# Kernel tuning notes

Measured on AMD Instinct MI355X. Metric: run time of the kernel, lower is better.

Reference implementation:

```python
import jax, jax.numpy as jnp
import numpy as np

KERNEL = 3
PAD = (KERNEL - 1) // 2
KA = KERNEL * KERNEL          # kernel_area = 9
CENTER = KA // 2              # 4
CH_OUT = 64


def setup_inputs() -> dict:
    key = jax.random.key(0)
    k1, k2 = jax.random.split(key)
    x = jax.random.normal(k1, (8, 64, 128, 128), dtype=jnp.float32)
    weight = jax.random.uniform(k2, (1, 1, KA, 1, 1), dtype=jnp.float32)
    bias = jnp.zeros((1, 1, KA, 1, 1), dtype=jnp.float32)
    weight_center = jnp.ones((), dtype=jnp.float32)
    weight_median = jnp.ones((), dtype=jnp.float32)
    return {"x": x, "weight": weight, "bias": bias,
            "weight_center": weight_center, "weight_median": weight_median}


def _unfold_same(x):
    # x: (B, C, H, W) -> patches (B, C, KA, H, W), stride 1, zero pad
    B, C, H, W = x.shape
    xp = jnp.pad(x, ((0, 0), (0, 0), (PAD, PAD), (PAD, PAD)))
    # order matches F.unfold: index = ki*K + kj
    views = [xp[:, :, i:i + H, j:j + W] for i in range(KERNEL) for j in range(KERNEL)]
    return jnp.stack(views, axis=2)


def reference(x, weight, bias, weight_center, weight_median):
    B, C, H, W = x.shape
    x_sig = jax.nn.sigmoid(x)
    patches = _unfold_same(x_sig)                      # (B, C, KA, H, W)
    w = jax.nn.sigmoid(weight)
    b = jax.nn.sigmoid(bias)
    D = jnp.maximum(w, patches) + b                    # (B, C, KA, H, W)
    max_stat = jnp.sum(D, axis=2)
    # torch.median returns the lower middle element -> sort and index (KA-1)//2
    median_stat = jnp.sort(D, axis=2)[:, :, (KA - 1) // 2]
    mean_stat = jnp.mean(D, axis=2)
    center = patches[:, :, CENTER]
    out = (weight_center * center + weight_median * median_stat
           - max_stat - mean_stat)                     # (B, C, H, W)
    # expand to ch_out then sum over C_in -> every output channel is identical
    s = jnp.sum(out, axis=1)                           # (B, H, W)
    return jnp.broadcast_to(s[:, None], (B, CH_OUT, H, W))
```

## Files before the change

kernel.cpp:

```cpp
#include <hip/hip_runtime.h>

#define BATCH  8
#define CH     64
#define H      128
#define W      128
#define HW     (H * W)
#define RS     8
#define CPW    2
#define NCHUNK (CH / CPW)
#define NSTRIP (H / RS)

typedef float vfloat2 __attribute__((ext_vector_type(2)));
typedef float vfloat4 __attribute__((ext_vector_type(4)));

__device__ __forceinline__ float sigmoidf_(float v) {
    return 1.0f / (1.0f + __expf(-v));
}

__device__ __forceinline__ float pixel_val(
    const float p0, const float p1, const float p2,
    const float p3, const float p4, const float p5,
    const float p6, const float p7, const float p8,
    const float* __restrict__ wk, const float* __restrict__ bk,
    const float wc, const float wm)
{
    float d[9];
    d[0] = fmaxf(wk[0], p0) + bk[0];
    d[1] = fmaxf(wk[1], p1) + bk[1];
    d[2] = fmaxf(wk[2], p2) + bk[2];
    d[3] = fmaxf(wk[3], p3) + bk[3];
    d[4] = fmaxf(wk[4], p4) + bk[4];
    d[5] = fmaxf(wk[5], p5) + bk[5];
    d[6] = fmaxf(wk[6], p6) + bk[6];
    d[7] = fmaxf(wk[7], p7) + bk[7];
    d[8] = fmaxf(wk[8], p8) + bk[8];
    float sum = ((d[0] + d[1]) + (d[2] + d[3])) + ((d[5] + d[6]) + (d[7] + d[8])) + d[4];

    #define S2(a,bb) { float t = d[a]; d[a] = fminf(d[a], d[bb]); d[bb] = fmaxf(t, d[bb]); }
    S2(0,3) S2(1,4) S2(2,5) S2(0,1) S2(0,2) S2(4,5) S2(3,5)
    S2(1,2) S2(3,4) S2(1,3) S2(1,6) S2(4,6) S2(2,6)
    S2(2,3) S2(4,7) S2(2,4) S2(3,7)
    S2(4,8) S2(3,8) S2(3,4)
    #undef S2

    return wc * p4 + wm * d[4] - sum - sum * (1.0f / 9.0f);
}

__global__ __launch_bounds__(256) void partial_kernel(
    const float* __restrict__ x,
    const float* __restrict__ weight,
    const float* __restrict__ bias,
    const float* __restrict__ wcp,
    const float* __restrict__ wmp,
    float* __restrict__ ws)
{
    const int tid   = threadIdx.x;
    const int lane  = tid & 63;
    const int strip = blockIdx.x * 4 + (tid >> 6);
    const int chnk  = blockIdx.y;
    const int c0    = chnk * CPW;
    const int b     = blockIdx.z;

    const int row0 = strip * RS;
    const int col  = 2 * lane;

    float wk[9], bk[9];
    #pragma unroll
    for (int k = 0; k < 9; ++k) {
        wk[k] = sigmoidf_(weight[k]);
        bk[k] = sigmoidf_(bias[k]);
    }
    const float wc = wcp[0];
    const float wm = wmp[0];

    vfloat2 raw[CPW][RS + 2];
    #pragma unroll
    for (int cc = 0; cc < CPW; ++cc) {
        const float* base = x + ((size_t)b * CH + c0 + cc) * HW + col;
        #pragma unroll
        for (int rr = 0; rr < RS + 2; ++rr) {
            const int r_  = row0 + rr - 1;
            const int rcl = min(max(r_, 0), H - 1);
            raw[cc][rr] = *(const vfloat2*)(base + rcl * W);
        }
    }

    vfloat2 acc[RS];
    #pragma unroll
    for (int j = 0; j < RS; ++j) acc[j] = (vfloat2)(0.0f);

    #define SIGROW(cc, rr, Lr, Ar, Br, Rr)                                    \
    {                                                                         \
        const int  r_  = row0 + (rr) - 1;                                     \
        const bool okr = (r_ >= 0) & (r_ < H);                                \
        vfloat2 v = raw[cc][rr];                                              \
        Ar = okr ? sigmoidf_(v.x) : 0.0f;                                     \
        Br = okr ? sigmoidf_(v.y) : 0.0f;                                     \
        float lf = __shfl_up(Br, 1);                                          \
        float rg = __shfl_down(Ar, 1);                                        \
        Lr = (lane == 0)  ? 0.0f : lf;                                        \
        Rr = (lane == 63) ? 0.0f : rg;                                        \
    }

    #pragma unroll
    for (int cc = 0; cc < CPW; ++cc) {
        float L0, A0, B0, R0, L1, A1, B1, R1, L2, A2, B2, R2;
        SIGROW(cc, 0, L0, A0, B0, R0);
        SIGROW(cc, 1, L1, A1, B1, R1);

        #pragma unroll
        for (int j = 0; j < RS; ++j) {
            SIGROW(cc, j + 2, L2, A2, B2, R2);

            acc[j].x += pixel_val(L0, A0, B0,
                                  L1, A1, B1,
                                  L2, A2, B2, wk, bk, wc, wm);
            acc[j].y += pixel_val(A0, B0, R0,
                                  A1, B1, R1,
                                  A2, B2, R2, wk, bk, wc, wm);

            L0 = L1; A0 = A1; B0 = B1; R0 = R1;
            L1 = L2; A1 = A2; B1 = B2; R1 = R2;
        }
    }
    #undef SIGROW

    float* op = ws + ((size_t)b * NCHUNK + chnk) * HW + (size_t)row0 * W + col;
    #pragma unroll
    for (int j = 0; j < RS; ++j)
        *(vfloat2*)(op + (size_t)j * W) = acc[j];
}

__global__ __launch_bounds__(256) void broadcast_kernel(
    const float* __restrict__ ws,
    float* __restrict__ out)
{
    const int g  = (blockIdx.x * 256 + threadIdx.x) * 4;
    const int b  = g >> 14;
    const int p  = g & (HW - 1);
    const int c0 = blockIdx.y * 16;

    const float* wsb = ws + (size_t)b * NCHUNK * HW + p;
    vfloat4 s = (vfloat4)(0.0f);
    #pragma unroll
    for (int k = 0; k < NCHUNK; ++k)
        s += *(const vfloat4*)(wsb + (size_t)k * HW);

    float* base = out + ((size_t)b * CH + c0) * HW + p;
    #pragma unroll
    for (int j = 0; j < 16; ++j)
        __builtin_nontemporal_store(s, (vfloat4*)(base + (size_t)j * HW));
}

extern "C" void kernel_launch(void* const* d_in, const int* in_sizes, int n_in,
                              void* d_out, int out_size, void* d_ws, size_t ws_size,
                              hipStream_t stream) {
    const float* x      = (const float*)d_in[0];
    const float* weight = (const float*)d_in[1];
    const float* bias   = (const float*)d_in[2];
    const float* wcp    = (const float*)d_in[3];
    const float* wmp    = (const float*)d_in[4];
    float* out = (float*)d_out;
    float* ws  = (float*)d_ws;

    dim3 grid1(NSTRIP / 4, NCHUNK, BATCH);
    partial_kernel<<<grid1, 256, 0, stream>>>(x, weight, bias, wcp, wmp, ws);

    dim3 grid2(BATCH * HW / (4 * 256), CH / 16);
    broadcast_kernel<<<grid2, 256, 0, stream>>>(ws, out);
}
```

Baseline: 111.6 us.

## Reduce channel partials in shared memory to shrink workspace traffic

Each 512-thread block now has 8 waves, each covering 4 channels over a 4-row strip. The per-wave partial sums are reduced across waves in LDS, so only 2 partial planes per batch go to the workspace instead of 32. This cuts workspace writes and the broadcast kernel's reads, and the broadcast grid is retuned to 8 channels per block. The cost is a block-wide sync, more halo rows reloaded and re-sigmoided per output row (6 loads for 4 rows versus 10 for 8), and higher register pressure from 4 channels of raw data per thread.

```diff
diff --git a/kernel.cpp b/kernel.cpp
--- a/kernel.cpp
+++ b/kernel.cpp
@@ -5,10 +5,10 @@
 #define H      128
 #define W      128
 #define HW     (H * W)
-#define RS     8
-#define CPW    2
-#define NCHUNK (CH / CPW)
-#define NSTRIP (H / RS)
+#define TH     4
+#define NSTRIP (H / TH)
+#define WAVES  8
+#define CPW    4
 
 typedef float vfloat2 __attribute__((ext_vector_type(2)));
 typedef float vfloat4 __attribute__((ext_vector_type(4)));
@@ -46,7 +46,7 @@
     return wc * p4 + wm * d[4] - sum - sum * (1.0f / 9.0f);
 }
 
-__global__ __launch_bounds__(256) void partial_kernel(
+__global__ __launch_bounds__(512) void partial_kernel(
     const float* __restrict__ x,
     const float* __restrict__ weight,
     const float* __restrict__ bias,
@@ -54,15 +54,18 @@
     const float* __restrict__ wmp,
     float* __restrict__ ws)
 {
-    const int tid   = threadIdx.x;
-    const int lane  = tid & 63;
-    const int strip = blockIdx.x * 4 + (tid >> 6);
-    const int chnk  = blockIdx.y;
-    const int c0    = chnk * CPW;
+    __shared__ float red[WAVES][TH][W];
+
+    const int tid  = threadIdx.x;
+    const int lane = tid & 63;
+    const int w    = tid >> 6;
+    const int strip = blockIdx.x;
+    const int half  = blockIdx.y;
     const int b     = blockIdx.z;
 
-    const int row0 = strip * RS;
+    const int row0 = strip * TH;
     const int col  = 2 * lane;
+    const int c0   = half * (WAVES * CPW) + w * CPW;
 
     float wk[9], bk[9];
     #pragma unroll
@@ -73,21 +76,21 @@
     const float wc = wcp[0];
     const float wm = wmp[0];
 
-    vfloat2 raw[CPW][RS + 2];
+    vfloat2 raw[CPW][TH + 2];
     #pragma unroll
     for (int cc = 0; cc < CPW; ++cc) {
         const float* base = x + ((size_t)b * CH + c0 + cc) * HW + col;
         #pragma unroll
-        for (int rr = 0; rr < RS + 2; ++rr) {
+        for (int rr = 0; rr < TH + 2; ++rr) {
             const int r_  = row0 + rr - 1;
             const int rcl = min(max(r_, 0), H - 1);
             raw[cc][rr] = *(const vfloat2*)(base + rcl * W);
         }
     }
 
-    vfloat2 acc[RS];
+    vfloat2 acc[TH];
     #pragma unroll
-    for (int j = 0; j < RS; ++j) acc[j] = (vfloat2)(0.0f);
+    for (int j = 0; j < TH; ++j) acc[j] = (vfloat2)(0.0f);
 
     #define SIGROW(cc, rr, Lr, Ar, Br, Rr)                                    \
     {                                                                         \
@@ -109,7 +112,7 @@
         SIGROW(cc, 1, L1, A1, B1, R1);
 
         #pragma unroll
-        for (int j = 0; j < RS; ++j) {
+        for (int j = 0; j < TH; ++j) {
             SIGROW(cc, j + 2, L2, A2, B2, R2);
 
             acc[j].x += pixel_val(L0, A0, B0,
@@ -125,10 +128,19 @@
     }
     #undef SIGROW
 
-    float* op = ws + ((size_t)b * NCHUNK + chnk) * HW + (size_t)row0 * W + col;
     #pragma unroll
-    for (int j = 0; j < RS; ++j)
-        *(vfloat2*)(op + (size_t)j * W) = acc[j];
+    for (int j = 0; j < TH; ++j)
+        *(vfloat2*)&red[w][j][col] = acc[j];
+    __syncthreads();
+
+    const int r  = tid >> 7;
+    const int cx = tid & 127;
+    float s = 0.0f;
+    #pragma unroll
+    for (int w2 = 0; w2 < WAVES; ++w2)
+        s += red[w2][r][cx];
+
+    ws[((size_t)b * 2 + half) * HW + (size_t)(row0 + r) * W + cx] = s;
 }
 
 __global__ __launch_bounds__(256) void broadcast_kernel(
@@ -138,18 +150,15 @@
     const int g  = (blockIdx.x * 256 + threadIdx.x) * 4;
     const int b  = g >> 14;
     const int p  = g & (HW - 1);
-    const int c0 = blockIdx.y * 16;
+    const int c0 = blockIdx.y * 8;
 
-    const float* wsb = ws + (size_t)b * NCHUNK * HW + p;
-    vfloat4 s = (vfloat4)(0.0f);
-    #pragma unroll
-    for (int k = 0; k < NCHUNK; ++k)
-        s += *(const vfloat4*)(wsb + (size_t)k * HW);
+    vfloat4 v = *(const vfloat4*)(ws + ((size_t)b * 2 + 0) * HW + p)
+              + *(const vfloat4*)(ws + ((size_t)b * 2 + 1) * HW + p);
 
     float* base = out + ((size_t)b * CH + c0) * HW + p;
     #pragma unroll
-    for (int j = 0; j < 16; ++j)
-        __builtin_nontemporal_store(s, (vfloat4*)(base + (size_t)j * HW));
+    for (int j = 0; j < 8; ++j)
+        __builtin_nontemporal_store(v, (vfloat4*)(base + (size_t)j * HW));
 }
 
 extern "C" void kernel_launch(void* const* d_in, const int* in_sizes, int n_in,
@@ -163,9 +172,9 @@
     float* out = (float*)d_out;
     float* ws  = (float*)d_ws;
 
-    dim3 grid1(NSTRIP / 4, NCHUNK, BATCH);
-    partial_kernel<<<grid1, 256, 0, stream>>>(x, weight, bias, wcp, wmp, ws);
+    dim3 grid1(NSTRIP, 2, BATCH);
+    partial_kernel<<<grid1, 512, 0, stream>>>(x, weight, bias, wcp, wmp, ws);
 
-    dim3 grid2(BATCH * HW / (4 * 256), CH / 16);
+    dim3 grid2(BATCH * HW / (4 * 256), CH / 8);
     broadcast_kernel<<<grid2, 256, 0, stream>>>(ws, out);
 }
```

Measured after the change: 121.2 us. +8.6%, slower.
